# Optimization experiments

Measured on AMD Instinct MI355X. Metric: run time of the kernel, lower is better.

Reference implementation:

```python
import jax, jax.numpy as jnp
import numpy as np

IN_CH, OUT_CH, K, UP = 512, 256, 3, 2
WSCALE = float(1.0 / np.sqrt(K * K * IN_CH))  # use_wscale gain / sqrt(fan_in), lr_mul=1
ACT_GAIN = float(np.sqrt(2.0))                # lrelu def_gain
CLAMP = 256.0                                  # conv_clamp * runtime_gain(=1)
FIR_PAD = 1                                    # px0+pxt = px1+pxt = 1 (derived in forward)

def _fir_filter():
    # upfirdn2d.setup_filter([1,3,3,1]): outer product then normalize to sum 1
    f1 = jnp.array([1.0, 3.0, 3.0, 1.0], jnp.float32)
    f2 = jnp.outer(f1, f1)
    return f2 / jnp.sum(f2)  # (4,4), sums to 1

def setup_inputs() -> dict:
    key = jax.random.key(0)
    k1, k2 = jax.random.split(key)
    return {
        "x": jax.random.normal(k1, (16, IN_CH, 64, 64), jnp.float32),
        "weight": jax.random.normal(k2, (OUT_CH, IN_CH, K, K), jnp.float32),
        "bias": jnp.zeros((OUT_CH,), jnp.float32),
    }

def _forward(x, weight, bias):
    w = weight * WSCALE  # runtime weight scaling
    # torch conv_transpose2d(x, w.transpose(0,1), stride=UP, padding=0)
    # == lhs-dilated correlation with spatially flipped kernel, pad K-1 each side
    k = w[:, :, ::-1, ::-1]
    y = jax.lax.conv_general_dilated(
        x, k, window_strides=(1, 1),
        padding=((K - 1, K - 1), (K - 1, K - 1)),
        lhs_dilation=(UP, UP),
        dimension_numbers=('NCHW', 'OIHW', 'NCHW'))  # (N, OUT_CH, 129, 129)
    # upfirdn2d(up=1, padding=(1,1,1,1), gain=UP**2):
    # pad, then depthwise conv with flipped filter scaled by gain**(ndim/2)=UP*UP
    f = _fir_filter() * (UP * UP)
    y = jnp.pad(y, ((0, 0), (0, 0), (FIR_PAD, FIR_PAD), (FIR_PAD, FIR_PAD)))
    fk = jnp.broadcast_to(f[::-1, ::-1][None, None], (OUT_CH, 1, 4, 4))
    y = jax.lax.conv_general_dilated(
        y, fk, (1, 1), 'VALID',
        feature_group_count=OUT_CH,
        dimension_numbers=('NCHW', 'OIHW', 'NCHW'))  # (N, OUT_CH, 128, 128)
    # bias_act: bias add, leaky_relu(0.2), gain sqrt(2), clamp +-256
    y = y + bias[None, :, None, None]
    y = jnp.where(y >= 0, y, 0.2 * y) * ACT_GAIN
    return jnp.clip(y, -CLAMP, CLAMP)

def reference(x, weight, bias):
    return _forward(x, weight, bias)
```

## Files before the change

kernel.cpp:

```cpp
#include <hip/hip_runtime.h>
#include <hip/hip_bf16.h>

#define NIMG 16
#define IN_CH 512
#define OUT_CH 256
#define HIN 64
#define HOUT 128
#define HP 66

#define WSCALE 0.014731391f
#define ACT_GAIN 1.41421356237f
#define CLAMP_V 256.0f

typedef __attribute__((ext_vector_type(8))) short bf16x8;
typedef __attribute__((ext_vector_type(4))) float f32x4;
typedef __attribute__((ext_vector_type(16))) float f32x16;

__device__ __constant__ float c_G[2][3][3] = {
    {{0.00f, 0.25f, 0.75f}, {0.75f, 0.75f, 0.25f}, {0.25f, 0.00f, 0.00f}},
    {{0.00f, 0.00f, 0.25f}, {0.25f, 0.75f, 0.75f}, {0.75f, 0.25f, 0.00f}}
};

#define XBF_BYTES ((size_t)NIMG * HP * HP * IN_CH * 2)
#define EBF_BYTES ((size_t)9 * 1024 * IN_CH * 2)
#define WS_NEED (XBF_BYTES + EBF_BYTES)

__global__ __launch_bounds__(256) void xpose_kernel(const float* __restrict__ x,
                                                    __hip_bfloat16* __restrict__ xbf) {
    const int n = blockIdx.z;
    const int hp = blockIdx.y;
    const int c0 = blockIdx.x << 6;
    const int tid = threadIdx.x;
    const size_t obase = ((size_t)n * HP + hp) * HP;

    if (hp == 0 || hp == HP - 1) {
        for (int idx = tid; idx < HP * 64; idx += 256) {
            int wp = idx >> 6, c = idx & 63;
            xbf[(obase + wp) * IN_CH + c0 + c] = __float2bfloat16(0.f);
        }
        return;
    }
    __shared__ float tile[64][65];
    {
        int cc = tid >> 6, w = tid & 63;
        for (int cb = 0; cb < 64; cb += 4)
            tile[cb + cc][w] =
                x[(((size_t)n * IN_CH + c0 + cb + cc) * HIN + (hp - 1)) * HIN + w];
    }
    __syncthreads();
    {
        int c = tid & 63, wg = tid >> 6;
        for (int wb = 0; wb < 64; wb += 4) {
            int w2 = wb + wg;
            xbf[(obase + (w2 + 1)) * IN_CH + c0 + c] = __float2bfloat16(tile[c][w2]);
        }
        if (tid < 128) {
            int which = tid >> 6, c2 = tid & 63;
            xbf[(obase + (which ? (HP - 1) : 0)) * IN_CH + c0 + c2] = __float2bfloat16(0.f);
        }
    }
}

__global__ __launch_bounds__(256) void build_ebf_kernel(const float* __restrict__ w,
                                                        __hip_bfloat16* __restrict__ ebf) {
    int gid = blockIdx.x * 256 + threadIdx.x;
    if (gid >= OUT_CH * IN_CH) return;
    int oc = gid >> 9, c = gid & 511;
    float wm[3][3];
    const float* wp = w + (size_t)gid * 9;
#pragma unroll
    for (int a = 0; a < 3; ++a)
#pragma unroll
        for (int b = 0; b < 3; ++b) wm[a][b] = wp[a * 3 + b] * WSCALE;
#pragma unroll
    for (int i = 0; i < 3; ++i)
#pragma unroll
        for (int j = 0; j < 3; ++j)
#pragma unroll
            for (int pu = 0; pu < 2; ++pu)
#pragma unroll
                for (int pv = 0; pv < 2; ++pv) {
                    float s = 0.f;
#pragma unroll
                    for (int a = 0; a < 3; ++a)
#pragma unroll
                        for (int b = 0; b < 3; ++b)
                            s += wm[a][b] * c_G[pu][i][a] * c_G[pv][j][b];
                    ebf[((size_t)(i * 3 + j) * 1024 + oc * 4 + pu * 2 + pv) * IN_CH + c] =
                        __float2bfloat16(s);
                }
}

#define MFMA8(AF, BF, MH)                                                                   \
    do {                                                                                    \
        acc[(MH)*4+0] = __builtin_amdgcn_mfma_f32_32x32x16_bf16((AF)[0], (BF)[0], acc[(MH)*4+0], 0, 0, 0); \
        acc[(MH)*4+1] = __builtin_amdgcn_mfma_f32_32x32x16_bf16((AF)[0], (BF)[2], acc[(MH)*4+1], 0, 0, 0); \
        acc[(MH)*4+2] = __builtin_amdgcn_mfma_f32_32x32x16_bf16((AF)[2], (BF)[0], acc[(MH)*4+2], 0, 0, 0); \
        acc[(MH)*4+3] = __builtin_amdgcn_mfma_f32_32x32x16_bf16((AF)[2], (BF)[2], acc[(MH)*4+3], 0, 0, 0); \
        acc[(MH)*4+0] = __builtin_amdgcn_mfma_f32_32x32x16_bf16((AF)[1], (BF)[1], acc[(MH)*4+0], 0, 0, 0); \
        acc[(MH)*4+1] = __builtin_amdgcn_mfma_f32_32x32x16_bf16((AF)[1], (BF)[3], acc[(MH)*4+1], 0, 0, 0); \
        acc[(MH)*4+2] = __builtin_amdgcn_mfma_f32_32x32x16_bf16((AF)[3], (BF)[1], acc[(MH)*4+2], 0, 0, 0); \
        acc[(MH)*4+3] = __builtin_amdgcn_mfma_f32_32x32x16_bf16((AF)[3], (BF)[3], acc[(MH)*4+3], 0, 0, 0); \
    } while (0)

#define CDA 270336
#define CDB 65536
#define DAK1(PAR) (((((PAR) ^ 1) << 2) | 1) << 14)
#define DBK1(PAR) (((((PAR) ^ 1) << 2) | 3) << 14)
#define DAK0(PAR) ((((PAR) << 2) | 0) << 14)
#define DBK0(PAR) ((((PAR) << 2) | 2) << 14)

#define GLL(SRC, DSTOFF)                                                          \
    __builtin_amdgcn_global_load_lds(                                             \
        (const __attribute__((address_space(1))) unsigned int*)(SRC),             \
        (__attribute__((address_space(3))) unsigned int*)(ldsW + (DSTOFF)), 16, 0, 0)

#define TILE_ITER(PAR, TT, SP01, SP23, VMS, LGK3, LAST)                           \
    {                                                                             \
        const int A0 = (PAR) ? aM0O : aM0E;                                       \
        const int A1 = (PAR) ? aM1O : aM1E;                                       \
        const int B0 = (PAR) ? bN0O : bN0E;                                       \
        const int B1 = (PAR) ? bN1O : bN1E;                                       \
        \
        afO[0] = *(const bf16x8*)&lds[A0 + 1024];                                 \
        afO[1] = *(const bf16x8*)&lds[A0 + 1024 + 8192];                          \
        afO[2] = *(const bf16x8*)&lds[A1 + 1024];                                 \
        afO[3] = *(const bf16x8*)&lds[A1 + 1024 + 8192];                          \
        if (SP01) { GLL(xbc + sA1 + voffA, DAK1(PAR));                            \
                    GLL(xbc + sA1 + voffA + CDA, DAK1(PAR) + 1024); }             \
        sA1 += ((TT) == 22 || (TT) == 46) ? 64640 : 128;                          \
        asm volatile("s_waitcnt lgkmcnt(4)" ::: "memory");                        \
        __builtin_amdgcn_sched_barrier(0);                                        \
        __builtin_amdgcn_s_setprio(1);                                            \
        MFMA8(afE, b0, 0);                                                        \
        __builtin_amdgcn_s_setprio(0);                                            \
        asm volatile("s_waitcnt " VMS ::: "memory");                              \
        __builtin_amdgcn_s_barrier();                                             \
        __builtin_amdgcn_sched_barrier(0);                                        \
          \
        afE[0] = *(const bf16x8*)&lds[A0 + 16384];                                \
        afE[1] = *(const bf16x8*)&lds[A0 + 16384 + 8192];                         \
        afE[2] = *(const bf16x8*)&lds[A1 + 16384];                                \
        afE[3] = *(const bf16x8*)&lds[A1 + 16384 + 8192];                         \
        b1[0] = *(const bf16x8*)&lds[B0 + 16384];                                 \
        b1[1] = *(const bf16x8*)&lds[B0 + 16384 + 8192];                          \
        b1[2] = *(const bf16x8*)&lds[B1 + 16384];                                 \
        b1[3] = *(const bf16x8*)&lds[B1 + 16384 + 8192];                          \
        if (SP01) { GLL(ebc + sB1 + voffB, DBK1(PAR));                            \
                    GLL(ebc + sB1 + voffB + CDB, DBK1(PAR) + 1024); }             \
        sB1 += (((TT) & 7) == 6) ? 1047680 : 128;                                 \
        asm volatile("s_waitcnt lgkmcnt(8)" ::: "memory");                        \
        __builtin_amdgcn_sched_barrier(0);                                        \
        __builtin_amdgcn_s_setprio(1);                                            \
        MFMA8(afO, b0, 1);                                                        \
        __builtin_amdgcn_s_setprio(0);                                            \
        __builtin_amdgcn_s_barrier();                                             \
        __builtin_amdgcn_sched_barrier(0);                                        \
        \
        afO[0] = *(const bf16x8*)&lds[A0 + 16384 + 1024];                         \
        afO[1] = *(const bf16x8*)&lds[A0 + 16384 + 1024 + 8192];                  \
        afO[2] = *(const bf16x8*)&lds[A1 + 16384 + 1024];                         \
        afO[3] = *(const bf16x8*)&lds[A1 + 16384 + 1024 + 8192];                  \
        if (SP23) { GLL(xbc + sA0 + voffA, DAK0(PAR));                            \
                    GLL(xbc + sA0 + voffA + CDA, DAK0(PAR) + 1024); }             \
        sA0 += ((TT) == 21 || (TT) == 45) ? 64640 : 128;                          \
        asm volatile("s_waitcnt lgkmcnt(4)" ::: "memory");                        \
        __builtin_amdgcn_sched_barrier(0);                                        \
        __builtin_amdgcn_s_setprio(1);                                            \
        MFMA8(afE, b1, 0);                                                        \
        __builtin_amdgcn_s_setprio(0);                                            \
        asm volatile("s_waitcnt " VMS ::: "memory");                              \
        __builtin_amdgcn_s_barrier();                                             \
        __builtin_amdgcn_sched_barrier(0);                                        \
           \
        if (!(LAST)) {                                                            \
            const int nA0 = (PAR) ? aM0E : aM0O;                                  \
            const int nA1 = (PAR) ? aM1E : aM1O;                                  \
            const int nB0 = (PAR) ? bN0E : bN0O;                                  \
            const int nB1 = (PAR) ? bN1E : bN1O;                                  \
            afE[0] = *(const bf16x8*)&lds[nA0];                                   \
            afE[1] = *(const bf16x8*)&lds[nA0 + 8192];                            \
            afE[2] = *(const bf16x8*)&lds[nA1];                                   \
            afE[3] = *(const bf16x8*)&lds[nA1 + 8192];                            \
            b0[0] = *(const bf16x8*)&lds[nB0];                                    \
            b0[1] = *(const bf16x8*)&lds[nB0 + 8192];                             \
            b0[2] = *(const bf16x8*)&lds[nB1];                                    \
            b0[3] = *(const bf16x8*)&lds[nB1 + 8192];                             \
        }                                                                         \
        if (SP23) { GLL(ebc + sB0 + voffB, DBK0(PAR));                            \
                    GLL(ebc + sB0 + voffB + CDB, DBK0(PAR) + 1024); }             \
        sB0 += (((TT) & 7) == 5) ? 1047680 : 128;                                 \
        asm volatile("s_waitcnt " LGK3 ::: "memory");                             \
        __builtin_amdgcn_sched_barrier(0);                                        \
        __builtin_amdgcn_s_setprio(1);                                            \
        MFMA8(afO, b1, 1);                                                        \
        __builtin_amdgcn_s_setprio(0);                                            \
        __builtin_amdgcn_s_barrier();                                             \
        __builtin_amdgcn_sched_barrier(0);                                        \
    }

__global__ __launch_bounds__(512, 2) void mfma_conv8_kernel(
    const __hip_bfloat16* __restrict__ xbf, const __hip_bfloat16* __restrict__ ebf,
    const float* __restrict__ bias, float* __restrict__ out) {
    __shared__ __align__(16) char lds[131072];

    const int tid = threadIdx.x;
    const int lane = tid & 63;
    const int wid = tid >> 6;
    const int wy = wid >> 2;
    const int wx = wid & 3;

    const int bid = blockIdx.x;
    const int wkid = ((bid & 7) << 7) + (bid >> 3);
    const int mtile = wkid >> 2;
    const int ntile = wkid & 3;
    const int n = mtile >> 4;
    const int sub = mtile & 15;
    const int qh0 = (sub >> 2) << 4;
    const int qw0 = (sub & 3) << 4;
    const int n0 = ntile << 8;

    const int slice = wid & 3;
    const int rowhalf = wid >> 2;

    f32x16 acc[8];
#pragma unroll
    for (int j = 0; j < 8; ++j) acc[j] = (f32x16)(0.f);

    char* ldsW = lds + (slice << 12) + (rowhalf << 11);
    const char* xbc = (const char*)xbf;
    const char* ebc = (const char*)ebf;

    const int q = lane ^ ((lane & 32) ? 4 : 0) ^ ((slice & 1) ? 4 : 0);
    const int voffA =
        ((n * HP + qh0 + (rowhalf << 3) + (q >> 4)) * HP + qw0 + (q & 15)) * 1024 +
        (slice << 4);
    const int voffB = ((n0 + (rowhalf << 7) + q) << 10) + (slice << 4);

    auto stage = [&](int s) {
        const int tt2 = s >> 2;
        const int part = s & 3;
        const int mat = part & 1;
        const int kh = part >> 1;
        const int slot = (((tt2 & 1) << 2) | (mat << 1) | kh) << 14;
        const int scal = tt2 * 128 + kh * 64;
#pragma unroll
        for (int c = 0; c < 2; ++c) {
            const char* src = mat == 0 ? (xbc + voffA + scal + c * CDA)
                                       : (ebc + voffB + scal + c * CDB);
            __builtin_amdgcn_global_load_lds(
                (const __attribute__((address_space(1))) unsigned int*)src,
                (__attribute__((address_space(3))) unsigned int*)(ldsW + slot + c * 1024),
                16, 0, 0);
        }
    };

    const int sl = lane >> 5;
    const int l31 = lane & 31;
    const int sx = sl ? 64 : 0;
    const int aM0E = (sl << 12) + (wy << 11) + ((l31 << 4) ^ sx);
    const int aM1E = (sl << 12) + (wy << 11) + 512 + ((l31 << 4) ^ 64 ^ sx);
    const int aM0O = aM0E + 65536;
    const int aM1O = aM1E + 65536;
    const int bN0E = 32768 + (sl << 12) + (wx << 10) + ((l31 << 4) ^ sx);
    const int bN1E = 32768 + (sl << 12) + (wx << 10) + 512 + ((l31 << 4) ^ 64 ^ sx);
    const int bN0O = bN0E + 65536;
    const int bN1O = bN1E + 65536;

    int sA1 = 192, sA0 = 256, sB1 = 192, sB0 = 256;

#pragma unroll
    for (int s = 0; s < 6; ++s) stage(s);
    asm volatile("s_waitcnt vmcnt(8)" ::: "memory");
    __builtin_amdgcn_s_barrier();
    __builtin_amdgcn_sched_barrier(0);

    bf16x8 afE[4], afO[4], b0[4], b1[4];
    afE[0] = *(const bf16x8*)&lds[aM0E];
    afE[1] = *(const bf16x8*)&lds[aM0E + 8192];
    afE[2] = *(const bf16x8*)&lds[aM1E];
    afE[3] = *(const bf16x8*)&lds[aM1E + 8192];
    b0[0] = *(const bf16x8*)&lds[bN0E];
    b0[1] = *(const bf16x8*)&lds[bN0E + 8192];
    b0[2] = *(const bf16x8*)&lds[bN1E];
    b0[3] = *(const bf16x8*)&lds[bN1E + 8192];

#pragma unroll 1
    for (int tt = 0; tt < 68; tt += 2) {
        TILE_ITER(0, tt, 1, 1, "vmcnt(6)", "lgkmcnt(8)", 0);
        TILE_ITER(1, tt + 1, 1, 1, "vmcnt(6)", "lgkmcnt(8)", 0);
    }
    TILE_ITER(0, 68, 1, 1, "vmcnt(6)", "lgkmcnt(8)", 0);
    TILE_ITER(1, 69, 1, 1, "vmcnt(0)", "lgkmcnt(8)", 0);
    TILE_ITER(0, 70, 1, 0, "vmcnt(0)", "lgkmcnt(8)", 0);
    TILE_ITER(1, 71, 0, 0, "vmcnt(0)", "lgkmcnt(0)", 1);

    float bv[2];
#pragma unroll
    for (int nt = 0; nt < 2; ++nt)
        bv[nt] = bias[(n0 + (wx << 6) + (nt << 5) + l31) >> 2];
#pragma unroll
    for (int j = 0; j < 8; ++j) {
        const int mt = j >> 1, nt = j & 1;
        const int nn = n0 + (wx << 6) + (nt << 5) + l31;
        const int oc = nn >> 2, pu = (nn >> 1) & 1, pv = nn & 1;
#pragma unroll
        for (int v = 0; v < 16; ++v) {
            const int m = (wy << 7) + (mt << 5) + (v & 3) + ((v >> 2) << 3) + (sl << 2);
            const int qr = m >> 4, qc = m & 15;
            const int hb = 2 * (qh0 + qr), wb = 2 * (qw0 + qc);
            float val = acc[j][v] + bv[nt];
            val = (val >= 0.f ? val : 0.2f * val) * ACT_GAIN;
            val = fminf(fmaxf(val, -CLAMP_V), CLAMP_V);
            out[(((size_t)n * OUT_CH + oc) * HOUT + (hb + pu)) * HOUT + (wb + pv)] = val;
        }
    }
}

__global__ void build_e_kernel(const float* __restrict__ w, float* __restrict__ e_ws) {
    int gid = blockIdx.x * blockDim.x + threadIdx.x;
    if (gid >= OUT_CH * IN_CH) return;
    float wm[3][3];
    const float* wp = w + (size_t)gid * 9;
#pragma unroll
    for (int a = 0; a < 3; ++a)
#pragma unroll
        for (int b = 0; b < 3; ++b) wm[a][b] = wp[a * 3 + b] * WSCALE;
    float* op = e_ws + (size_t)gid * 36;
#pragma unroll
    for (int i = 0; i < 3; ++i)
#pragma unroll
        for (int j = 0; j < 3; ++j)
#pragma unroll
            for (int pu = 0; pu < 2; ++pu)
#pragma unroll
                for (int pv = 0; pv < 2; ++pv) {
                    float s = 0.f;
#pragma unroll
                    for (int a = 0; a < 3; ++a)
#pragma unroll
                        for (int b = 0; b < 3; ++b)
                            s += wm[a][b] * c_G[pu][i][a] * c_G[pv][j][b];
                    op[(i * 3 + j) * 4 + pu * 2 + pv] = s;
                }
}

#define OGB 8
#define CB 8
#define QT 16
__global__ __launch_bounds__(256) void fused_conv_kernel(
    const float* __restrict__ x, const float* __restrict__ e_ws,
    const float* __restrict__ bias, float* __restrict__ out) {
    __shared__ float sX[CB][18][19];
    __shared__ float4 sE[OGB * CB * 9];
    const int tid = threadIdx.x;
    const int o2 = tid >> 7;
    const int qy = (tid >> 3) & 15;
    const int qxp = tid & 7;
    const int tileIdx = blockIdx.x;
    const int hq0 = (tileIdx >> 2) * QT;
    const int wq0 = (tileIdx & 3) * QT;
    const int o0 = blockIdx.y * OGB;
    const int n = blockIdx.z;
    float4 acc[2][4];
#pragma unroll
    for (int q = 0; q < 2; ++q)
#pragma unroll
        for (int oo = 0; oo < 4; ++oo) acc[q][oo] = make_float4(0.f, 0.f, 0.f, 0.f);
    for (int c0 = 0; c0 < IN_CH; c0 += CB) {
        for (int idx = tid; idx < CB * 18 * 18; idx += 256) {
            int cc = idx / 324;
            int rem = idx - cc * 324;
            int r = rem / 18;
            int col = rem - r * 18;
            int h = hq0 - 1 + r;
            int ww = wq0 - 1 + col;
            float v = 0.f;
            if (h >= 0 && h < HIN && ww >= 0 && ww < HIN)
                v = x[(((size_t)n * IN_CH + (c0 + cc)) * HIN + h) * HIN + ww];
            sX[cc][r][col] = v;
        }
        {
            float* sEf = (float*)sE;
            for (int idx = tid; idx < OGB * CB * 36; idx += 256) {
                int ol = idx / (CB * 36);
                int rem = idx - ol * (CB * 36);
                sEf[ol * (CB * 36) + rem] =
                    e_ws[((size_t)(o0 + ol) * IN_CH + c0) * 36 + rem];
            }
        }
        __syncthreads();
#pragma unroll 1
        for (int cc = 0; cc < CB; ++cc) {
#pragma unroll
            for (int i = 0; i < 3; ++i) {
#pragma unroll
                for (int j = 0; j < 3; ++j) {
                    float xv0 = sX[cc][qy + i][2 * qxp + j];
                    float xv1 = sX[cc][qy + i][2 * qxp + 1 + j];
#pragma unroll
                    for (int oo = 0; oo < 4; ++oo) {
                        float4 e = sE[((o2 * 4 + oo) * CB + cc) * 9 + i * 3 + j];
                        acc[0][oo].x += xv0 * e.x; acc[0][oo].y += xv0 * e.y;
                        acc[0][oo].z += xv0 * e.z; acc[0][oo].w += xv0 * e.w;
                        acc[1][oo].x += xv1 * e.x; acc[1][oo].y += xv1 * e.y;
                        acc[1][oo].z += xv1 * e.z; acc[1][oo].w += xv1 * e.w;
                    }
                }
            }
        }
        __syncthreads();
    }
#pragma unroll
    for (int q = 0; q < 2; ++q) {
        int qx = 2 * qxp + q;
        int u0 = 2 * (hq0 + qy);
        int v0 = 2 * (wq0 + qx);
#pragma unroll
        for (int oo = 0; oo < 4; ++oo) {
            int o = o0 + o2 * 4 + oo;
            float b = bias[o];
            float vals[4] = {acc[q][oo].x, acc[q][oo].y, acc[q][oo].z, acc[q][oo].w};
#pragma unroll
            for (int p = 0; p < 4; ++p) {
                int pu = p >> 1, pv = p & 1;
                float v = vals[p] + b;
                v = (v >= 0.f ? v : 0.2f * v) * ACT_GAIN;
                v = fminf(fmaxf(v, -CLAMP_V), CLAMP_V);
                out[(((size_t)n * OUT_CH + o) * HOUT + (u0 + pu)) * HOUT + (v0 + pv)] = v;
            }
        }
    }
}

extern "C" void kernel_launch(void* const* d_in, const int* in_sizes, int n_in,
                              void* d_out, int out_size, void* d_ws, size_t ws_size,
                              hipStream_t stream) {
    const float* x = (const float*)d_in[0];
    const float* w = (const float*)d_in[1];
    const float* bias = (const float*)d_in[2];
    float* out = (float*)d_out;

    if (ws_size >= WS_NEED) {
        __hip_bfloat16* xbf = (__hip_bfloat16*)d_ws;
        __hip_bfloat16* ebf = (__hip_bfloat16*)((char*)d_ws + XBF_BYTES);
        xpose_kernel<<<dim3(8, HP, NIMG), 256, 0, stream>>>(x, xbf);
        build_ebf_kernel<<<(OUT_CH * IN_CH + 255) / 256, 256, 0, stream>>>(w, ebf);
        mfma_conv8_kernel<<<dim3(1024), 512, 0, stream>>>(xbf, ebf, bias, out);
    } else {
        float* e_ws = (float*)d_ws;
        build_e_kernel<<<(OUT_CH * IN_CH + 255) / 256, 256, 0, stream>>>(w, e_ws);
        dim3 grid(16, OUT_CH / OGB, NIMG);
        fused_conv_kernel<<<grid, 256, 0, stream>>>(x, e_ws, bias, out);
    }
}
```

Baseline: 735.3 us.

## Store activations and weights in channel-group-blocked layout for coalesced LDS loads

Changes the bf16 intermediate layouts for the padded input and the expanded weights. Channels are now split into 8-channel groups (16-byte chunks) placed outermost, instead of sitting contiguous in the innermost dimension. The transpose and weight-build kernels write the new layout, and the GEMM kernel's global-to-LDS address offsets and per-iteration stride updates are recomputed to match. The aim is that each wave's 16-byte global loads hit contiguous memory across lanes rather than being strided by 1 KB, which should improve coalescing and cache behaviour. The cost is less contiguous per-pixel stores in the transpose kernel and more complex offset arithmetic.

New measurement: 629.6 us. -14.4%, faster.

```diff
diff --git a/kernel.cpp b/kernel.cpp
--- a/kernel.cpp
+++ b/kernel.cpp
@@ -21,8 +21,8 @@
     {{0.00f, 0.00f, 0.25f}, {0.25f, 0.75f, 0.75f}, {0.75f, 0.25f, 0.00f}}
 };
 
-#define XBF_BYTES ((size_t)NIMG * HP * HP * IN_CH * 2)
-#define EBF_BYTES ((size_t)9 * 1024 * IN_CH * 2)
+#define XBF_BYTES ((size_t)NIMG * 64 * HP * HP * 16)
+#define EBF_BYTES ((size_t)9 * 64 * 1024 * 16)
 #define WS_NEED (XBF_BYTES + EBF_BYTES)
 
 __global__ __launch_bounds__(256) void xpose_kernel(const float* __restrict__ x,
@@ -31,12 +31,14 @@
     const int hp = blockIdx.y;
     const int c0 = blockIdx.x << 6;
     const int tid = threadIdx.x;
-    const size_t obase = ((size_t)n * HP + hp) * HP;
+    const int sgb = c0 >> 3;
+    const bf16x8 zero = {0, 0, 0, 0, 0, 0, 0, 0};
 
     if (hp == 0 || hp == HP - 1) {
-        for (int idx = tid; idx < HP * 64; idx += 256) {
-            int wp = idx >> 6, c = idx & 63;
-            xbf[(obase + wp) * IN_CH + c0 + c] = __float2bfloat16(0.f);
+        for (int idx = tid; idx < 8 * HP; idx += 256) {
+            int s3 = idx / HP, wp = idx - s3 * HP;
+            size_t a = (((size_t)(n * 64 + sgb + s3) * HP + hp) * HP + wp);
+            *(bf16x8*)((char*)xbf + a * 16) = zero;
         }
         return;
     }
@@ -49,14 +51,23 @@
     }
     __syncthreads();
     {
-        int c = tid & 63, wg = tid >> 6;
-        for (int wb = 0; wb < 64; wb += 4) {
-            int w2 = wb + wg;
-            xbf[(obase + (w2 + 1)) * IN_CH + c0 + c] = __float2bfloat16(tile[c][w2]);
-        }
-        if (tid < 128) {
-            int which = tid >> 6, c2 = tid & 63;
-            xbf[(obase + (which ? (HP - 1) : 0)) * IN_CH + c0 + c2] = __float2bfloat16(0.f);
+        int s3 = tid >> 5, wq = tid & 31;
+#pragma unroll
+        for (int wb = 0; wb < 64; wb += 32) {
+            int wimg = wb + wq;
+            bf16x8 v;
+#pragma unroll
+            for (int k = 0; k < 8; ++k) {
+                __hip_bfloat16 b = __float2bfloat16(tile[s3 * 8 + k][wimg]);
+                v[k] = *reinterpret_cast<short*>(&b);
+            }
+            size_t a = (((size_t)(n * 64 + sgb + s3) * HP + hp) * HP + (wimg + 1));
+            *(bf16x8*)((char*)xbf + a * 16) = v;
+        }
+        if (tid < 16) {
+            int s3h = tid >> 1, wph = (tid & 1) ? (HP - 1) : 0;
+            size_t a = (((size_t)(n * 64 + sgb + s3h) * HP + hp) * HP + wph);
+            *(bf16x8*)((char*)xbf + a * 16) = zero;
         }
     }
 }
@@ -66,6 +77,7 @@
     int gid = blockIdx.x * 256 + threadIdx.x;
     if (gid >= OUT_CH * IN_CH) return;
     int oc = gid >> 9, c = gid & 511;
+    int sg = c >> 3, ce = c & 7;
     float wm[3][3];
     const float* wp = w + (size_t)gid * 9;
 #pragma unroll
@@ -86,7 +98,8 @@
 #pragma unroll
                         for (int b = 0; b < 3; ++b)
                             s += wm[a][b] * c_G[pu][i][a] * c_G[pv][j][b];
-                    ebf[((size_t)(i * 3 + j) * 1024 + oc * 4 + pu * 2 + pv) * IN_CH + c] =
+                    int row = oc * 4 + pu * 2 + pv;
+                    ebf[(((size_t)(i * 3 + j) * 64 + sg) * 1024 + row) * 8 + ce] =
                         __float2bfloat16(s);
                 }
 }
@@ -103,8 +116,12 @@
         acc[(MH)*4+3] = __builtin_amdgcn_mfma_f32_32x32x16_bf16((AF)[3], (BF)[3], acc[(MH)*4+3], 0, 0, 0); \
     } while (0)
 
-#define CDA 270336
-#define CDB 65536
+#define CDA 4224
+#define CDB 1024
+#define ASTEP 557568
+#define AJ_FJ (-3902960)
+#define AJ_FI (-3901952)
+#define BSTEP 131072
 #define DAK1(PAR) (((((PAR) ^ 1) << 2) | 1) << 14)
 #define DBK1(PAR) (((((PAR) ^ 1) << 2) | 3) << 14)
 #define DAK0(PAR) ((((PAR) << 2) | 0) << 14)
@@ -128,7 +145,8 @@
         afO[3] = *(const bf16x8*)&lds[A1 + 1024 + 8192];                          \
         if (SP01) { GLL(xbc + sA1 + voffA, DAK1(PAR));                            \
                     GLL(xbc + sA1 + voffA + CDA, DAK1(PAR) + 1024); }             \
-        sA1 += ((TT) == 22 || (TT) == 46) ? 64640 : 128;                          \
+        sA1 += (((TT) & 7) == 6) ? (((TT) == 22 || (TT) == 46) ? AJ_FI : AJ_FJ)   \
+                                 : ASTEP;                                         \
         asm volatile("s_waitcnt lgkmcnt(4)" ::: "memory");                        \
         __builtin_amdgcn_sched_barrier(0);                                        \
         __builtin_amdgcn_s_setprio(1);                                            \
@@ -148,7 +166,7 @@
         b1[3] = *(const bf16x8*)&lds[B1 + 16384 + 8192];                          \
         if (SP01) { GLL(ebc + sB1 + voffB, DBK1(PAR));                            \
                     GLL(ebc + sB1 + voffB + CDB, DBK1(PAR) + 1024); }             \
-        sB1 += (((TT) & 7) == 6) ? 1047680 : 128;                                 \
+        sB1 += BSTEP;                                                             \
         asm volatile("s_waitcnt lgkmcnt(8)" ::: "memory");                        \
         __builtin_amdgcn_sched_barrier(0);                                        \
         __builtin_amdgcn_s_setprio(1);                                            \
@@ -163,7 +181,8 @@
         afO[3] = *(const bf16x8*)&lds[A1 + 16384 + 1024 + 8192];                  \
         if (SP23) { GLL(xbc + sA0 + voffA, DAK0(PAR));                            \
                     GLL(xbc + sA0 + voffA + CDA, DAK0(PAR) + 1024); }             \
-        sA0 += ((TT) == 21 || (TT) == 45) ? 64640 : 128;                          \
+        sA0 += (((TT) & 7) == 5) ? (((TT) == 21 || (TT) == 45) ? AJ_FI : AJ_FJ)   \
+                                 : ASTEP;                                         \
         asm volatile("s_waitcnt lgkmcnt(4)" ::: "memory");                        \
         __builtin_amdgcn_sched_barrier(0);                                        \
         __builtin_amdgcn_s_setprio(1);                                            \
@@ -189,7 +208,7 @@
         }                                                                         \
         if (SP23) { GLL(ebc + sB0 + voffB, DBK0(PAR));                            \
                     GLL(ebc + sB0 + voffB + CDB, DBK0(PAR) + 1024); }             \
-        sB0 += (((TT) & 7) == 5) ? 1047680 : 128;                                 \
+        sB0 += BSTEP;                                                             \
         asm volatile("s_waitcnt " LGK3 ::: "memory");                             \
         __builtin_amdgcn_sched_barrier(0);                                        \
         __builtin_amdgcn_s_setprio(1);                                            \
@@ -233,9 +252,9 @@
 
     const int q = lane ^ ((lane & 32) ? 4 : 0) ^ ((slice & 1) ? 4 : 0);
     const int voffA =
-        ((n * HP + qh0 + (rowhalf << 3) + (q >> 4)) * HP + qw0 + (q & 15)) * 1024 +
-        (slice << 4);
-    const int voffB = ((n0 + (rowhalf << 7) + q) << 10) + (slice << 4);
+        ((((n << 6) + slice) * HP + qh0 + (rowhalf << 3) + (q >> 4)) * HP + qw0 +
+         (q & 15)) * 16;
+    const int voffB = (slice << 14) + ((n0 + (rowhalf << 7) + q) << 4);
 
     auto stage = [&](int s) {
         const int tt2 = s >> 2;
@@ -243,11 +262,11 @@
         const int mat = part & 1;
         const int kh = part >> 1;
         const int slot = (((tt2 & 1) << 2) | (mat << 1) | kh) << 14;
-        const int scal = tt2 * 128 + kh * 64;
+        const int sgoff = (tt2 << 3) + (kh << 2);
 #pragma unroll
         for (int c = 0; c < 2; ++c) {
-            const char* src = mat == 0 ? (xbc + voffA + scal + c * CDA)
-                                       : (ebc + voffB + scal + c * CDB);
+            const char* src = mat == 0 ? (xbc + voffA + sgoff * 69696 + c * CDA)
+                                       : (ebc + voffB + sgoff * 16384 + c * CDB);
             __builtin_amdgcn_global_load_lds(
                 (const __attribute__((address_space(1))) unsigned int*)src,
                 (__attribute__((address_space(3))) unsigned int*)(ldsW + slot + c * 1024),
@@ -267,7 +286,10 @@
     const int bN0O = bN0E + 65536;
     const int bN1O = bN1E + 65536;
 
-    int sA1 = 192, sA0 = 256, sB1 = 192, sB0 = 256;
+    int sA1 = 12 * 69696;
+    int sA0 = 16 * 69696;
+    int sB1 = 12 * 16384;
+    int sB0 = 16 * 16384;
 
 #pragma unroll
     for (int s = 0; s < 6; ++s) stage(s);
```
